# Kernel optimization log

Measured on AMD Instinct MI355X. Metric: run time of the kernel, lower is better.

The kernel has to match this reference:

```python
import jax, jax.numpy as jnp
import numpy as np

B, L, D_MODEL, H, M = 16, 512, 512, 8, 2
E = D_MODEL // H      # d_keys = d_values = 64
KMA = 25              # series-decomp moving-average kernel
KLAM = 7              # lambda conv kernel in TrendRefinement
PI = float(np.pi)


def _diff_matrix(n):
    # first-order difference matrix, shape (n-1, n)
    D = np.zeros((n - 1, n), dtype=np.float32)
    D[:, 1:] += np.eye(n - 1, dtype=np.float32)
    D[:, :-1] -= np.eye(n - 1, dtype=np.float32)
    return D


def setup_inputs() -> dict:
    key = jax.random.key(0)
    ks = jax.random.split(key, 16)
    w = lambda k, shape, s=0.02: s * jax.random.normal(k, shape, dtype=jnp.float32)
    # TrendRefinement buffers: U,S from SVD of (D2^T D2), D2 = D_{L-1} @ D_L (second difference)
    D2 = _diff_matrix(L - 1) @ _diff_matrix(L)
    U, S, _ = np.linalg.svd(D2.T @ D2)
    return {
        'queries': jax.random.normal(ks[0], (B, L, D_MODEL), dtype=jnp.float32),
        'keys':    jax.random.normal(ks[1], (B, L, D_MODEL), dtype=jnp.float32),
        'values':  jax.random.normal(ks[2], (B, L, D_MODEL), dtype=jnp.float32),
        'Wq': w(ks[3], (D_MODEL, H * E)), 'bq': jnp.zeros((H * E,), jnp.float32),
        'Wk': w(ks[4], (D_MODEL, H * E)), 'bk': jnp.zeros((H * E,), jnp.float32),
        'Wv': w(ks[5], (D_MODEL, H * E)), 'bv': jnp.zeros((H * E,), jnp.float32),
        'Wqo': w(ks[6], (D_MODEL, M * H)), 'bqo': jnp.zeros((M * H,), jnp.float32),
        'Wko': w(ks[7], (D_MODEL, M * H)), 'bko': jnp.zeros((M * H,), jnp.float32),
        'Wqt': w(ks[8], (D_MODEL, M * H)), 'bqt': jnp.zeros((M * H,), jnp.float32),
        'Wkt': w(ks[9], (D_MODEL, M * H)), 'bkt': jnp.zeros((M * H,), jnp.float32),
        'Wo': w(ks[10], (H * E, D_MODEL)), 'bo': jnp.zeros((D_MODEL,), jnp.float32),
        'Wlam': w(ks[11], (1, E, KLAM), 0.1), 'blam': jnp.zeros((1,), jnp.float32),
        'U': jnp.asarray(U, dtype=jnp.float32),
        'S': jnp.asarray(S, dtype=jnp.float32),
    }


def _mov_avg(x):
    # x: (B, L, H, E); replicate-pad then window mean of size KMA, stride 1
    pad = (KMA - 1) // 2
    xp = jnp.concatenate([jnp.repeat(x[:, :1], pad, axis=1), x,
                          jnp.repeat(x[:, -1:], pad, axis=1)], axis=1)
    c = jnp.cumsum(xp, axis=1)
    c = jnp.concatenate([jnp.zeros_like(c[:, :1]), c], axis=1)
    return (c[:, KMA:] - c[:, :-KMA]) / jnp.float32(KMA)


def _forward(queries, keys, values, Wq, bq, Wk, bk, Wv, bv, Wqo, bqo, Wko, bko,
             Wqt, bqt, Wkt, bkt, Wo, bo, Wlam, blam, U, S):
    # phase (omega/theta) projections: kernel-1 Conv1d == pointwise linear
    q_om = jax.nn.relu(queries @ Wqo + bqo).reshape(B, L, H, M)
    k_om = jax.nn.relu(keys @ Wko + bko).reshape(B, L, H, M)
    q_th = jnp.tanh(queries @ Wqt + bqt).reshape(B, L, H, M) * PI
    k_th = jnp.tanh(keys @ Wkt + bkt).reshape(B, L, H, M) * PI

    q = (queries @ Wq + bq).reshape(B, L, H, E)
    k = (keys @ Wk + bk).reshape(B, L, H, E)
    v = (values @ Wv + bv).reshape(B, L, H, E)

    # series decomposition: keep residual, keep value trend
    q = q - _mov_avg(q)
    k = k - _mov_avg(k)
    v_trend = _mov_avg(v)
    v = v - v_trend

    # inner attention: periodic-rotation-modulated softmax attention
    t = jnp.arange(L, dtype=jnp.float32)[None, :, None, None]

    def rot(x, om, th):
        phase = om * t + th                                     # (B,L,H,M)
        c, s = jnp.cos(phase), jnp.sin(phase)
        xr = jnp.concatenate([x[..., None, :] * c[..., None],
                              x[..., None, :] * s[..., None]], axis=-1)  # (B,L,H,M,2E)
        return xr.reshape(B, L, H, 2 * M * E)

    qr = rot(q, q_om, q_th)
    kr = rot(k, k_om, k_th)
    scores = jnp.einsum('blhd,bshd->bhls', qr, kr) / jnp.sqrt(jnp.float32(E))
    attn = jax.nn.softmax(scores, axis=-1)
    out = jnp.einsum('bhls,bshd->blhd', attn, v)

    # trend refinement: per-(b,h) filter g = U diag(1/(1+lambda*S)) U^T
    pad = (KLAM - 1) // 2
    vt = v_trend.transpose(0, 2, 3, 1).reshape(B * H, E, L)
    vtp = jnp.pad(vt, ((0, 0), (0, 0), (pad, pad)), mode='edge')
    lam = jax.lax.conv_general_dilated(vtp, Wlam, (1,), 'VALID',
                                       dimension_numbers=('NCH', 'OIH', 'NCH'))
    lam = lam + blam[None, :, None]
    lambdas = 1.0 + jax.nn.elu(lam).reshape(B, H, L)            # lambdas[b,h,l]
    s_scaled = lambdas * S[None, None, :]                        # (B,H,L)
    g = jnp.einsum('il,bhl,jl->bhij', U, 1.0 / (1.0 + s_scaled), U)
    out = out + jnp.einsum('bhij,bjhd->bihd', g, v_trend)

    out = out.reshape(B, L, H * E) @ Wo + bo

    # smoothness penalties
    Dq = jnp.asarray(_diff_matrix(L))
    om_pen = (jnp.sum(jnp.einsum('ji,bihm->bjhm', Dq, q_om) ** 2)
              + jnp.sum(jnp.einsum('ji,bihm->bjhm', Dq, k_om) ** 2))
    th_pen = jnp.sum(q_th ** 2) + jnp.sum(k_th ** 2)
    return out, attn, om_pen, th_pen


def reference(queries, keys, values, Wq, bq, Wk, bk, Wv, bv, Wqo, bqo, Wko, bko,
              Wqt, bqt, Wkt, bkt, Wo, bo, Wlam, blam, U, S):
    return _forward(queries, keys, values, Wq, bq, Wk, bk, Wv, bv, Wqo, bqo,
                    Wko, bko, Wqt, bqt, Wkt, bkt, Wo, bo, Wlam, blam, U, S)
```

## Files before the change

kernel.cpp:

```cpp
#include <hip/hip_runtime.h>
#include <math.h>


#define PI_F 3.14159265358979323846f

typedef __attribute__((ext_vector_type(8))) short bf16x8;
typedef __attribute__((ext_vector_type(4))) float f32x4;

static constexpr long ATTN_OFF = 4194304;
static constexpr long OM_OFF   = 37748736;
static constexpr long TH_OFF   = 37748737;

__device__ __forceinline__ ushort f2bf(float f){
  uint u = __float_as_uint(f);
  u += 0x7fffu + ((u >> 16) & 1u);
  return (ushort)(u >> 16);
}
__device__ __forceinline__ float bf2f(ushort h){
  return __uint_as_float((uint)h << 16);
}
__device__ __forceinline__ uint4 cvt8s(const float* f){
  ushort h[8];
#pragma unroll
  for (int j = 0; j < 8; j++) h[j] = f2bf(f[j]);
  uint4 H;
  H.x = (uint)h[0] | ((uint)h[1] << 16); H.y = (uint)h[2] | ((uint)h[3] << 16);
  H.z = (uint)h[4] | ((uint)h[5] << 16); H.w = (uint)h[6] | ((uint)h[7] << 16);
  return H;
}

template<int ROWS>
__device__ __forceinline__ void stage_sb(const short* __restrict__ G, int ldk,
                                         short* dst, int t){
#pragma unroll
  for (int i = 0; i < ROWS*8/256; i++){
    int p = t + i*256;
    int row = p >> 3;
    int kb = (p & 7) ^ (row & 7);
    __builtin_amdgcn_global_load_lds(
        (const __attribute__((address_space(1))) uint*)(G + (long)row*ldk + kb*8),
        (__attribute__((address_space(3))) uint*)(dst + (long)p*8), 16, 0, 0);
  }
}

template<int ROWS>
__device__ __forceinline__ void stage_sync(const short* __restrict__ G, int ldk,
                                           short* dst, int t){
#pragma unroll
  for (int i = 0; i < ROWS*8/256; i++){
    int p = t + i*256;
    int row = p >> 3, kb = p & 7;
    uint4 v = *(const uint4*)(G + (long)row*ldk + kb*8);
    *(uint4*)&dst[row*64 + ((kb ^ (row & 7)) << 3)] = v;
  }
}

template<int BM,int BN,bool QKV,int EPI>
__global__ __launch_bounds__(256)
void mgemm(int K,
  const short* __restrict__ AB, int lda, long sAb, long sAh,
  const short* __restrict__ BB, long sBb, long sBh,
  float* __restrict__ C, int ldc, long sCb, long sCh,
  const float* __restrict__ bias, const float* __restrict__ bias1, const float* __restrict__ bias2,
  const float* __restrict__ wcolp, short* __restrict__ CB, int Hdiv)
{
  __shared__ short As[BM*64], Bs[BN*64];
  constexpr int WMT = BM/2, WNT = BN/2;
  constexpr int FM = WMT/16, FN = WNT/16;

  const int z = blockIdx.z;
  const int zb = z / Hdiv, zh = z % Hdiv;
  const short* Ab = AB;
  const short* Bb = BB;
  float* Cb = C;
  short* Cbb = CB;
  if constexpr (QKV){
    Ab += (long)zb*4194304;
    if constexpr (EPI >= 4) Cbb += (long)zb*4194304;
  } else {
    Ab += (long)zb*sAb + (long)zh*sAh;
    Bb += (long)zb*sBb + (long)zh*sBh;
    if (C) Cb += (long)zb*sCb + (long)zh*sCh;
    if constexpr (EPI >= 4) Cbb += (long)zb*sCb + (long)zh*sCh;
  }

  const int t = threadIdx.x;
  const int m0 = blockIdx.y*BM, n0 = blockIdx.x*BN;
  const int wave = t >> 6, lane = t & 63;
  const int wr = wave >> 1, wc = wave & 1;
  const int lr = lane & 15, lk = lane >> 4;

  f32x4 acc[FM][FN];
#pragma unroll
  for (int mi = 0; mi < FM; mi++)
#pragma unroll
    for (int nj = 0; nj < FN; nj++) acc[mi][nj] = (f32x4){0.f, 0.f, 0.f, 0.f};

  for (int k0 = 0; k0 < K; k0 += 64){
    stage_sb<BM>(Ab + (long)m0*lda + k0, lda, As, t);
    stage_sb<BN>(Bb + (long)n0*K + k0, K, Bs, t);
    __syncthreads();
#pragma unroll
    for (int kk = 0; kk < 2; kk++){
      bf16x8 ah[FM], bh[FN];
#pragma unroll
      for (int mi = 0; mi < FM; mi++){
        int row = wr*WMT + mi*16 + lr;
        ah[mi] = *(const bf16x8*)&As[row*64 + (((kk*4 + lk) ^ (row & 7)) << 3)];
      }
#pragma unroll
      for (int nj = 0; nj < FN; nj++){
        int col = wc*WNT + nj*16 + lr;
        bh[nj] = *(const bf16x8*)&Bs[col*64 + (((kk*4 + lk) ^ (col & 7)) << 3)];
      }
#pragma unroll
      for (int mi = 0; mi < FM; mi++)
#pragma unroll
        for (int nj = 0; nj < FN; nj++)
          acc[mi][nj] = __builtin_amdgcn_mfma_f32_16x16x32_bf16(ah[mi], bh[nj], acc[mi][nj], 0, 0, 0);
    }
    __syncthreads();
  }

  const float* wz = nullptr;
  if constexpr (EPI == 4) wz = wcolp + (long)z*512;
  const float* bp = bias;
  if constexpr (QKV) bp = (zb == 0) ? bias : ((zb == 1) ? bias1 : bias2);

#pragma unroll
  for (int mi = 0; mi < FM; mi++){
#pragma unroll
    for (int r = 0; r < 4; r++){
      int grow = m0 + wr*WMT + mi*16 + lk*4 + r;
#pragma unroll
      for (int nj = 0; nj < FN; nj++){
        int gcol = n0 + wc*WNT + nj*16 + lr;
        float v = acc[mi][nj][r];
        if constexpr (EPI == 1 || EPI == 6) v += bp[gcol];
        if constexpr (EPI == 5) v += Cb[(long)grow*ldc + gcol];
        if constexpr (EPI == 4) v *= wz[gcol];
        if constexpr (EPI >= 4) Cbb[(long)grow*ldc + gcol] = (short)f2bf(v);
        else                    Cb[(long)grow*ldc + gcol] = v;
      }
    }
  }
}

__global__ __launch_bounds__(256)
void wconv_t(const float* __restrict__ W0, const float* __restrict__ W1,
             const float* __restrict__ W2, const float* __restrict__ W3,
             short* B0, short* B1, short* B2, short* B3)
{
  const float* W; short* Bp;
  switch (blockIdx.z){
    case 0:  W = W0; Bp = B0; break;
    case 1:  W = W1; Bp = B1; break;
    case 2:  W = W2; Bp = B2; break;
    default: W = W3; Bp = B3; break;
  }
  __shared__ float s[64][65];
  const int r0 = blockIdx.y*64, c0 = blockIdx.x*64;
  const int t = threadIdx.x;
#pragma unroll
  for (int i = 0; i < 4; i++){
    int idx = t + i*256;
    int r = idx >> 4, c4 = (idx & 15)*4;
    float4 v = *(const float4*)(W + (long)(r0 + r)*512 + c0 + c4);
    s[r][c4+0] = v.x; s[r][c4+1] = v.y; s[r][c4+2] = v.z; s[r][c4+3] = v.w;
  }
  __syncthreads();
#pragma unroll
  for (int i = 0; i < 2; i++){
    int p = t + i*256;
    int n = p >> 3, kb = p & 7;
    float f[8];
#pragma unroll
    for (int j = 0; j < 8; j++) f[j] = s[kb*8 + j][n];
    *(uint4*)&Bp[(long)(c0 + n)*512 + r0 + kb*8] = cvt8s(f);
  }
}

__global__ __launch_bounds__(256)
void uconv(const float* __restrict__ U, short* __restrict__ UB, short* __restrict__ UtB)
{
  __shared__ float s[64][65];
  const int r0 = blockIdx.y*64, c0 = blockIdx.x*64;
  const int t = threadIdx.x;
#pragma unroll
  for (int i = 0; i < 4; i++){
    int idx = t + i*256;
    int r = idx >> 4, c4 = (idx & 15)*4;
    float4 v = *(const float4*)(U + (long)(r0 + r)*512 + c0 + c4);
    s[r][c4+0] = v.x; s[r][c4+1] = v.y; s[r][c4+2] = v.z; s[r][c4+3] = v.w;
  }
  __syncthreads();
#pragma unroll
  for (int i = 0; i < 2; i++){
    int p = t + i*256;
    int rr = p >> 3, kb = p & 7;
    float f[8];
#pragma unroll
    for (int j = 0; j < 8; j++) f[j] = s[rr][kb*8 + j];
    *(uint4*)&UB[(long)(r0 + rr)*512 + c0 + kb*8] = cvt8s(f);
  }
#pragma unroll
  for (int i = 0; i < 2; i++){
    int p = t + i*256;
    int n = p >> 3, kb = p & 7;
    float f[8];
#pragma unroll
    for (int j = 0; j < 8; j++) f[j] = s[kb*8 + j][n];
    *(uint4*)&UtB[(long)(c0 + n)*512 + r0 + kb*8] = cvt8s(f);
  }
}

__global__ __launch_bounds__(256)
void acvt(const float* __restrict__ q, const float* __restrict__ k,
          const float* __restrict__ v, short* __restrict__ base)
{
  long g = (long)blockIdx.x*256 + threadIdx.x;
  if (g >= 1572864) return;
  long idx = g & 524287; int sel = (int)(g >> 19);
  const float* src = sel == 0 ? q : (sel == 1 ? k : v);
  short* Bp = base + (long)sel*4194304;
  float f[8];
  *(float4*)&f[0] = *(const float4*)(src + idx*8);
  *(float4*)&f[4] = *(const float4*)(src + idx*8 + 4);
  *(uint4*)&Bp[idx*8] = cvt8s(f);
}

__global__ __launch_bounds__(256)
void skinny_k(const float* __restrict__ Xq, const float* __restrict__ Xk,
              const float* __restrict__ Wqo, const float* __restrict__ bqo,
              const float* __restrict__ Wqt, const float* __restrict__ bqt,
              const float* __restrict__ Wko, const float* __restrict__ bko,
              const float* __restrict__ Wkt, const float* __restrict__ bkt,
              float* __restrict__ q_om, float* __restrict__ q_th, float* __restrict__ Cq,
              float* __restrict__ k_om, float* __restrict__ k_th, float* __restrict__ Ck)
{
    const int sel = blockIdx.y;
    const float* X   = sel ? Xk  : Xq;
    const float* Wom = sel ? Wko : Wqo;  const float* bom = sel ? bko : bqo;
    const float* Wth = sel ? Wkt : Wqt;  const float* bth = sel ? bkt : bqt;
    float* om_out = sel ? k_om : q_om;
    float* th_out = sel ? k_th : q_th;
    float* Cph    = sel ? Ck   : Cq;

    const int t = threadIdx.x;
    const int tx = t & 31, ty = t >> 5;
    const long row = (long)blockIdx.x * 8 + ty;
    const int col = tx & 15;
    const bool isTh = tx >= 16;
    const float* __restrict__ Wm = isTh ? Wth : Wom;
    const float* __restrict__ xr = X + row * 512;
    float acc0 = 0.f, acc1 = 0.f, acc2 = 0.f, acc3 = 0.f;
    for (int k = 0; k < 512; k += 4) {
        acc0 += xr[k + 0] * Wm[(k + 0) * 16 + col];
        acc1 += xr[k + 1] * Wm[(k + 1) * 16 + col];
        acc2 += xr[k + 2] * Wm[(k + 2) * 16 + col];
        acc3 += xr[k + 3] * Wm[(k + 3) * 16 + col];
    }
    float acc = (acc0 + acc1) + (acc2 + acc3);
    __shared__ float som[8][16], sth[8][16];
    float res;
    if (isTh) {
        res = tanhf(acc + bth[col]) * PI_F;
        th_out[row * 16 + col] = res;
        sth[ty][col] = res;
    } else {
        res = fmaxf(acc + bom[col], 0.f);
        om_out[row * 16 + col] = res;
        som[ty][col] = res;
    }
    __syncthreads();
    if (t < 64){
        const int r2 = t >> 3, h = t & 7;
        const long grow = (long)blockIdx.x * 8 + r2;
        const float tt = (float)(grow & 511);
        const float o0 = som[r2][h*2], o1 = som[r2][h*2+1];
        const float t0 = sth[r2][h*2], t1 = sth[r2][h*2+1];
        float c0, s0, c1, s1;
        sincosf(o0 * tt + t0, &s0, &c0);
        sincosf(o1 * tt + t1, &s1, &c1);
        float4 rr = { c0, s0, c1, s1 };
        *(float4*)&Cph[grow * 32 + h * 4] = rr;
    }
}

__global__ __launch_bounds__(256)
void movavg_all(const short* __restrict__ qpB, const short* __restrict__ kpB,
                const short* __restrict__ vpB,
                short* __restrict__ qRB, short* __restrict__ kRB,
                short* __restrict__ VTB, short* __restrict__ TTB)
{
    const int zz = blockIdx.z;
    const int src = zz >> 4, b = zz & 15;
    const int l0 = blockIdx.y * 64, c0 = blockIdx.x * 64;
    const short* XB = src == 0 ? qpB : (src == 1 ? kpB : vpB);
    short* RB = src == 0 ? qRB : kRB;
    __shared__ float sm[88][64];
    const long base = (long)b * 512 * 512 + c0;
    const int t = threadIdx.x;
    for (int i = t; i < 88 * 64; i += 256) {
        const int r = i >> 6, c = i & 63;
        int gl = l0 + r - 12;
        gl = min(max(gl, 0), 511);
        sm[r][c] = bf2f((ushort)XB[base + (long)gl * 512 + c]);
    }
    __syncthreads();
    const int tx = t & 63, ty = t >> 6;
    const int rbase = ty * 16;
    float s = 0.f;
    #pragma unroll
    for (int d = 0; d < 25; d++) s += sm[rbase + d][tx];
    const float inv = 1.f / 25.f;
    short hb[16], tb[16];
    #pragma unroll
    for (int r = 0; r < 16; r++) {
        const long l = l0 + rbase + r;
        const float ma = s * inv;
        const float x = sm[rbase + r + 12][tx];
        const float res = x - ma;
        if (src < 2) {
            RB[((long)b * 512 + l) * 512 + c0 + tx] = (short)f2bf(res);
        } else {
            hb[r] = (short)f2bf(res);
            tb[r] = (short)f2bf(ma);
        }
        if (r < 15) s += sm[rbase + r + 25][tx] - sm[rbase + r][tx];
    }
    if (src == 2) {
        const long vo = ((long)b * 512 + c0 + tx) * 512 + l0 + rbase;
        *(uint4*)&VTB[vo]     = ((uint4*)hb)[0];
        *(uint4*)&VTB[vo + 8] = ((uint4*)hb)[1];
        *(uint4*)&TTB[vo]     = ((uint4*)tb)[0];
        *(uint4*)&TTB[vo + 8] = ((uint4*)tb)[1];
    }
}

__global__ __launch_bounds__(256)
void flash_k(const short* __restrict__ qB, const short* __restrict__ kB,
             const short* __restrict__ vtB,
             const float* __restrict__ Cq, const float* __restrict__ Ck,
             float* __restrict__ attn, float* __restrict__ attn_out)
{
  const int bid = blockIdx.y*8 + blockIdx.x;
  const int swz = (bid & 7)*128 + (bid >> 3);
  const int z = swz >> 3; const int b = z >> 3, h = z & 7;
  const int l0 = (swz & 7) * 64;
  const int t = threadIdx.x, wave = t >> 6, lane = t & 63;
  const int lr = lane & 15, lk = lane >> 4;

  __shared__ short SH[8192];
  __shared__ float CkS[2048];
  short* Qs = SH;
  short* Ks = SH;
  short* PPs = SH;
  short* Vs = SH + 4096;

  const int sr0 = t >> 3,          skb0 = t & 7;
  const int sr1 = (t >> 3) + 32,   skb1 = t & 7;
  const int sidx0 = sr0*64 + ((skb0 ^ (sr0 & 7)) << 3);
  const int sidx1 = sr1*64 + ((skb1 ^ (sr1 & 7)) << 3);

  stage_sync<64>(qB + ((long)(b*512 + l0))*512 + h*64, 512, Qs, t);
#pragma unroll
  for (int i = 0; i < 2; i++){
    int s = t + i*256;
    ((float4*)CkS)[s] = *(const float4*)(Ck + (((long)b*512 + s)*8 + h)*4);
  }
  __syncthreads();
  bf16x8 aq[2];
#pragma unroll
  for (int kk = 0; kk < 2; kk++){
    int row = wave*16 + lr;
    aq[kk] = *(const bf16x8*)&Qs[row*64 + (((kk*4 + lk) ^ (row & 7)) << 3)];
  }

  const long kbase0 = ((long)(b*512 + sr0))*512 + h*64 + skb0*8;
  const long kbase1 = ((long)(b*512 + sr1))*512 + h*64 + skb1*8;
  uint4 pA0, pA1, pB0, pB1;
  pA0 = *(const uint4*)(kB + kbase0);
  pA1 = *(const uint4*)(kB + kbase1);
  __syncthreads();

  f32x4 acc[32];
#pragma unroll
  for (int a = 0; a < 32; a++) acc[a] = (f32x4){0.f,0.f,0.f,0.f};
#pragma unroll
  for (int st = 0; st < 8; st++){
    if (st & 1){
      *(uint4*)&Ks[sidx0] = pB0; *(uint4*)&Ks[sidx1] = pB1;
      if (st < 7){
        pA0 = *(const uint4*)(kB + kbase0 + (long)(st+1)*64*512);
        pA1 = *(const uint4*)(kB + kbase1 + (long)(st+1)*64*512);
      }
    } else {
      *(uint4*)&Ks[sidx0] = pA0; *(uint4*)&Ks[sidx1] = pA1;
      if (st < 7){
        pB0 = *(const uint4*)(kB + kbase0 + (long)(st+1)*64*512);
        pB1 = *(const uint4*)(kB + kbase1 + (long)(st+1)*64*512);
      }
    }
    __syncthreads();
#pragma unroll
    for (int nj = 0; nj < 4; nj++){
      int srow = nj*16 + lr;
#pragma unroll
      for (int kk = 0; kk < 2; kk++){
        bf16x8 bh = *(const bf16x8*)&Ks[srow*64 + (((kk*4 + lk) ^ (srow & 7)) << 3)];
        acc[st*4+nj] = __builtin_amdgcn_mfma_f32_16x16x32_bf16(aq[kk], bh, acc[st*4+nj], 0,0,0);
      }
    }
    if (st < 7) __syncthreads();
  }

  const long vbase0 = ((long)(z*64 + sr0))*512 + skb0*8;
  const long vbase1 = ((long)(z*64 + sr1))*512 + skb1*8;
  pA0 = *(const uint4*)(vtB + vbase0);
  pA1 = *(const uint4*)(vtB + vbase1);

  float4 cqv[4];
#pragma unroll
  for (int r = 0; r < 4; r++){
    int row = l0 + wave*16 + lk*4 + r;
    cqv[r] = *(const float4*)(Cq + (((long)b*512 + row)*8 + h)*4);
  }
#pragma unroll
  for (int a = 0; a < 32; a++){
    int col = (a >> 2)*64 + (a & 3)*16 + lr;
    float4 ckv = ((float4*)CkS)[col];
#pragma unroll
    for (int r = 0; r < 4; r++){
      float mod = 0.125f*(cqv[r].x*ckv.x + cqv[r].y*ckv.y + cqv[r].z*ckv.z + cqv[r].w*ckv.w);
      acc[a][r] *= mod;
    }
  }
  float mx[4] = {-INFINITY, -INFINITY, -INFINITY, -INFINITY};
#pragma unroll
  for (int a = 0; a < 32; a++)
#pragma unroll
    for (int r = 0; r < 4; r++) mx[r] = fmaxf(mx[r], acc[a][r]);
#pragma unroll
  for (int msk = 1; msk < 16; msk <<= 1)
#pragma unroll
    for (int r = 0; r < 4; r++) mx[r] = fmaxf(mx[r], __shfl_xor(mx[r], msk));
  float sme[4] = {0.f, 0.f, 0.f, 0.f};
#pragma unroll
  for (int a = 0; a < 32; a++)
#pragma unroll
    for (int r = 0; r < 4; r++){ float e = __expf(acc[a][r] - mx[r]); acc[a][r] = e; sme[r] += e; }
#pragma unroll
  for (int msk = 1; msk < 16; msk <<= 1)
#pragma unroll
    for (int r = 0; r < 4; r++) sme[r] += __shfl_xor(sme[r], msk);
  float inv[4];
#pragma unroll
  for (int r = 0; r < 4; r++) inv[r] = 1.f / sme[r];
#pragma unroll
  for (int a = 0; a < 32; a++)
#pragma unroll
    for (int r = 0; r < 4; r++) acc[a][r] *= inv[r];

  f32x4 oacc[4];
#pragma unroll
  for (int nj = 0; nj < 4; nj++) oacc[nj] = (f32x4){0.f,0.f,0.f,0.f};
#pragma unroll
  for (int st = 0; st < 8; st++){
    __syncthreads();
#pragma unroll
    for (int a2 = 0; a2 < 4; a2++){
      int c = a2*16 + lr;
#pragma unroll
      for (int r = 0; r < 4; r++){
        int row = wave*16 + lk*4 + r;
        PPs[row*64 + (((c >> 3) ^ (row & 7)) << 3) + (c & 7)] = (short)f2bf(acc[st*4+a2][r]);
      }
    }
    if (st & 1){
      *(uint4*)&Vs[sidx0] = pB0; *(uint4*)&Vs[sidx1] = pB1;
      if (st < 7){
        pA0 = *(const uint4*)(vtB + vbase0 + (st+1)*64);
        pA1 = *(const uint4*)(vtB + vbase1 + (st+1)*64);
      }
    } else {
      *(uint4*)&Vs[sidx0] = pA0; *(uint4*)&Vs[sidx1] = pA1;
      if (st < 7){
        pB0 = *(const uint4*)(vtB + vbase0 + (st+1)*64);
        pB1 = *(const uint4*)(vtB + vbase1 + (st+1)*64);
      }
    }
#pragma unroll
    for (int a2 = 0; a2 < 4; a2++){
      int col = st*64 + a2*16 + lr;
#pragma unroll
      for (int r = 0; r < 4; r++)
        attn[((long)z*512 + l0 + wave*16 + lk*4 + r)*512 + col] = acc[st*4+a2][r];
    }
    __syncthreads();
#pragma unroll
    for (int kk = 0; kk < 2; kk++){
      int prow = wave*16 + lr;
      int phys = (kk*4 + lk) ^ (prow & 7);
      bf16x8 ah = *(const bf16x8*)&PPs[prow*64 + phys*8];
#pragma unroll
      for (int nj = 0; nj < 4; nj++){
        int vrow = nj*16 + lr;
        bf16x8 bh = *(const bf16x8*)&Vs[vrow*64 + (((kk*4 + lk) ^ (vrow & 7)) << 3)];
        oacc[nj] = __builtin_amdgcn_mfma_f32_16x16x32_bf16(ah, bh, oacc[nj], 0,0,0);
      }
    }
  }
#pragma unroll
  for (int nj = 0; nj < 4; nj++)
#pragma unroll
    for (int r = 0; r < 4; r++){
      int grow = l0 + wave*16 + lk*4 + r;
      attn_out[((long)b*512 + grow)*512 + h*64 + nj*16 + lr] = oacc[nj][r];
    }
}

__global__ __launch_bounds__(512)
void lamw_k(const short* __restrict__ TTB, const float* __restrict__ Wlam,
            const float* __restrict__ blam, const float* __restrict__ Sv,
            float* __restrict__ Wout)
{
    const int z = blockIdx.x;
    const int b = z >> 3, h = z & 7;
    __shared__ float sv[512][17];
    __shared__ float sw[448];
    const int t = threadIdx.x;
    if (t < 448) sw[t] = Wlam[t];
    const short* __restrict__ Tb = TTB + ((long)b * 512 + h * 64) * 512;
    float lam = 0.f;
    for (int ec = 0; ec < 4; ec++) {
        __syncthreads();
        #pragma unroll
        for (int j = 0; j < 16; j++)
            sv[t][j] = bf2f((ushort)Tb[(long)(ec * 16 + j) * 512 + t]);
        __syncthreads();
        #pragma unroll
        for (int dk = 0; dk < 7; dk++) {
            int r = t + dk - 3;
            r = min(max(r, 0), 511);
            #pragma unroll
            for (int j = 0; j < 16; j++)
                lam += sv[r][j] * sw[(ec * 16 + j) * 7 + dk];
        }
    }
    lam += blam[0];
    const float el = lam > 0.f ? lam : expm1f(lam);
    const float wv = 1.f / (1.f + (1.f + el) * Sv[t]);
    Wout[(long)z * 512 + t] = wv;
}

__global__ __launch_bounds__(256)
void pen1_k(const float* __restrict__ qom, const float* __restrict__ kom,
            const float* __restrict__ qth, const float* __restrict__ kth,
            float* __restrict__ partials)
{
    const long tid = (long)blockIdx.x * 256 + threadIdx.x;
    float om = 0.f, th = 0.f;
    for (long i = tid; i < 262144; i += 65536) {
        const float* om_arr = (i < 131072) ? qom : kom;
        const float* th_arr = (i < 131072) ? qth : kth;
        const long j = i & 131071;
        const float x = th_arr[j];
        th += x * x;
        const int l = (int)((j >> 4) & 511);
        if (l < 511) {
            const float d = om_arr[j + 16] - om_arr[j];
            om += d * d;
        }
    }
    __shared__ float som[256], sth[256];
    som[threadIdx.x] = om; sth[threadIdx.x] = th;
    __syncthreads();
    for (int o = 128; o; o >>= 1) {
        if (threadIdx.x < o) {
            som[threadIdx.x] += som[threadIdx.x + o];
            sth[threadIdx.x] += sth[threadIdx.x + o];
        }
        __syncthreads();
    }
    if (threadIdx.x == 0) {
        partials[blockIdx.x] = som[0];
        partials[256 + blockIdx.x] = sth[0];
    }
}

__global__ __launch_bounds__(256)
void pen2_k(const float* __restrict__ partials, float* __restrict__ om_out,
            float* __restrict__ th_out)
{
    __shared__ float som[256], sth[256];
    const int t = threadIdx.x;
    som[t] = partials[t]; sth[t] = partials[256 + t];
    __syncthreads();
    for (int o = 128; o; o >>= 1) {
        if (t < o) { som[t] += som[t + o]; sth[t] += sth[t + o]; }
        __syncthreads();
    }
    if (t == 0) { *om_out = som[0]; *th_out = sth[0]; }
}

extern "C" void kernel_launch(void* const* d_in, const int* in_sizes, int n_in,
                              void* d_out_v, int out_size, void* d_ws, size_t ws_size,
                              hipStream_t stream)
{
    const float* queries = (const float*)d_in[0];
    const float* keys    = (const float*)d_in[1];
    const float* values  = (const float*)d_in[2];
    const float* Wq  = (const float*)d_in[3];  const float* bq  = (const float*)d_in[4];
    const float* Wk  = (const float*)d_in[5];  const float* bk  = (const float*)d_in[6];
    const float* Wv  = (const float*)d_in[7];  const float* bv  = (const float*)d_in[8];
    const float* Wqo = (const float*)d_in[9];  const float* bqo = (const float*)d_in[10];
    const float* Wko = (const float*)d_in[11]; const float* bko = (const float*)d_in[12];
    const float* Wqt = (const float*)d_in[13]; const float* bqt = (const float*)d_in[14];
    const float* Wkt = (const float*)d_in[15]; const float* bkt = (const float*)d_in[16];
    const float* Wo  = (const float*)d_in[17]; const float* bo  = (const float*)d_in[18];
    const float* Wlam= (const float*)d_in[19]; const float* blam= (const float*)d_in[20];
    const float* U   = (const float*)d_in[21]; const float* Sv  = (const float*)d_in[22];

    float* out = (float*)d_out_v;
    float* W   = (float*)d_ws;

    short* qpB = (short*)W;
    short* kpB = (short*)(W + 4194304);
    short* vpB = (short*)(W + 8388608);
    float* attn_out = W + 4194304;
    short* TTB = (short*)(W + 12582912);
    short* R1  = (short*)(W + 16777216);
    short* qinB = R1;
    short* kinB = R1 + 4194304;
    short* vinB = R1 + 8388608;
    short* qresB = qinB;  short* kresB = kinB;  short* vtB = vinB;
    short* aoB = kresB;
    short* T1tB = (short*)W;
    short* UB  = (short*)(W + 8388608);
    short* UtB = UB + 262144;
    float* q_om = W + 29360128;
    float* k_om = q_om + 131072;
    float* q_th = k_om + 131072;
    float* k_th = q_th + 131072;
    float* Cq   = k_th + 131072;
    float* Ck   = Cq + 262144;
    float* wbuf = Ck + 262144;
    float* partials = wbuf + 65536;
    short* wsp = (short*)(W + 30475264);
    short* WqB = wsp;
    short* WkB = wsp + 262144;
    short* WvB = wsp + 524288;
    short* WoB = wsp + 786432;

    float* attn = out + ATTN_OFF;
    dim3 blk(256);

    wconv_t<<<dim3(8,8,4), blk, 0, stream>>>(Wq, Wk, Wv, Wo, WqB, WkB, WvB, WoB);
    acvt<<<dim3(6144), blk, 0, stream>>>(queries, keys, values, R1);

    mgemm<128,128,true,6><<<dim3(4,64,3), blk, 0, stream>>>(
        512, qinB, 512, 0, 0, WqB, 0, 0,
        nullptr, 512, 0, 0,
        bq, bk, bv, nullptr, qpB, 1);

    skinny_k<<<dim3(1024,2), blk, 0, stream>>>(queries, keys,
        Wqo, bqo, Wqt, bqt, Wko, bko, Wkt, bkt,
        q_om, q_th, Cq, k_om, k_th, Ck);

    movavg_all<<<dim3(8,8,48), blk, 0, stream>>>(qpB, kpB, vpB,
        qresB, kresB, vtB, TTB);

    uconv<<<dim3(8,8), blk, 0, stream>>>(U, UB, UtB);

    flash_k<<<dim3(8,128), blk, 0, stream>>>(qresB, kresB, vtB, Cq, Ck, attn, attn_out);

    lamw_k<<<dim3(128), dim3(512), 0, stream>>>(TTB, Wlam, blam, Sv, wbuf);

    mgemm<64,128,false,4><<<dim3(4,1,128), blk, 0, stream>>>(
        512, TTB, 512, 262144, 32768, UtB, 0, 0,
        nullptr, 512, 262144, 32768,
        nullptr, nullptr, nullptr, wbuf, T1tB, 8);

    mgemm<128,64,false,5><<<dim3(1,4,128), blk, 0, stream>>>(
        512, UB, 512, 0, 0, T1tB, 262144, 32768,
        attn_out, 512, 262144, 64,
        nullptr, nullptr, nullptr, nullptr, aoB, 8);

    mgemm<64,128,false,1><<<dim3(4,128,1), blk, 0, stream>>>(
        512, aoB, 512, 0, 0, WoB, 0, 0,
        out, 512, 0, 0,
        bo, nullptr, nullptr, nullptr, nullptr, 1);

    pen1_k<<<dim3(256), blk, 0, stream>>>(q_om, k_om, q_th, k_th, partials);
    pen2_k<<<dim3(1), blk, 0, stream>>>(partials, out + OM_OFF, out + TH_OFF);
}
```

Baseline: 240.1 us.

## Double-buffer K/P/V tiles in LDS with 128-wide stages and MFMA priority

The flash attention kernel now processes keys and values in four stages of 128 instead of eight of 64. K, P and V tiles are double-buffered in LDS, which removes one barrier per stage, and the swizzle moves from the LDS write side to the global read side. s_setprio is raised around the MFMA loops. LDS use grows from about 24KB to about 72KB per block, which may reduce occupancy, and more prefetch registers are live.

```diff
diff --git a/kernel.cpp b/kernel.cpp
--- a/kernel.cpp
+++ b/kernel.cpp
@@ -351,17 +351,15 @@
   const int t = threadIdx.x, wave = t >> 6, lane = t & 63;
   const int lr = lane & 15, lk = lane >> 4;
 
-  __shared__ short SH[8192];
+  __shared__ short SH[32768];
   __shared__ float CkS[2048];
-  short* Qs = SH;
-  short* Ks = SH;
-  short* PPs = SH;
-  short* Vs = SH + 4096;
-
-  const int sr0 = t >> 3,          skb0 = t & 7;
-  const int sr1 = (t >> 3) + 32,   skb1 = t & 7;
-  const int sidx0 = sr0*64 + ((skb0 ^ (sr0 & 7)) << 3);
-  const int sidx1 = sr1*64 + ((skb1 ^ (sr1 & 7)) << 3);
+  short* Qs  = SH;
+  short* Ks0 = SH;
+  short* Ks1 = SH + 8192;
+  short* PP0 = SH;
+  short* PP1 = SH + 8192;
+  short* Vs0 = SH + 16384;
+  short* Vs1 = SH + 24576;
 
   stage_sync<64>(qB + ((long)(b*512 + l0))*512 + h*64, 512, Qs, t);
 #pragma unroll
@@ -377,48 +375,65 @@
     aq[kk] = *(const bf16x8*)&Qs[row*64 + (((kk*4 + lk) ^ (row & 7)) << 3)];
   }
 
-  const long kbase0 = ((long)(b*512 + sr0))*512 + h*64 + skb0*8;
-  const long kbase1 = ((long)(b*512 + sr1))*512 + h*64 + skb1*8;
-  uint4 pA0, pA1, pB0, pB1;
-  pA0 = *(const uint4*)(kB + kbase0);
-  pA1 = *(const uint4*)(kB + kbase1);
+  int sidx[4]; long kgoff[4];
+  uint4 pA0,pA1,pA2,pA3, pB0,pB1,pB2,pB3;
+#pragma unroll
+  for (int i = 0; i < 4; i++){
+    int p = t + i*256;
+    int row = p >> 3, kb = p & 7;
+    sidx[i] = p*8;
+    kgoff[i] = ((long)(b*512 + row))*512 + h*64 + ((kb ^ (row & 7))*8);
+  }
+  pA0 = *(const uint4*)(kB + kgoff[0]); pA1 = *(const uint4*)(kB + kgoff[1]);
+  pA2 = *(const uint4*)(kB + kgoff[2]); pA3 = *(const uint4*)(kB + kgoff[3]);
   __syncthreads();
 
   f32x4 acc[32];
 #pragma unroll
   for (int a = 0; a < 32; a++) acc[a] = (f32x4){0.f,0.f,0.f,0.f};
 #pragma unroll
-  for (int st = 0; st < 8; st++){
+  for (int st = 0; st < 4; st++){
+    short* Kcur = (st & 1) ? Ks1 : Ks0;
     if (st & 1){
-      *(uint4*)&Ks[sidx0] = pB0; *(uint4*)&Ks[sidx1] = pB1;
-      if (st < 7){
-        pA0 = *(const uint4*)(kB + kbase0 + (long)(st+1)*64*512);
-        pA1 = *(const uint4*)(kB + kbase1 + (long)(st+1)*64*512);
+      *(uint4*)&Kcur[sidx[0]] = pB0; *(uint4*)&Kcur[sidx[1]] = pB1;
+      *(uint4*)&Kcur[sidx[2]] = pB2; *(uint4*)&Kcur[sidx[3]] = pB3;
+      if (st < 3){
+        long o = (long)(st+1)*128*512;
+        pA0 = *(const uint4*)(kB + kgoff[0] + o); pA1 = *(const uint4*)(kB + kgoff[1] + o);
+        pA2 = *(const uint4*)(kB + kgoff[2] + o); pA3 = *(const uint4*)(kB + kgoff[3] + o);
       }
     } else {
-      *(uint4*)&Ks[sidx0] = pA0; *(uint4*)&Ks[sidx1] = pA1;
-      if (st < 7){
-        pB0 = *(const uint4*)(kB + kbase0 + (long)(st+1)*64*512);
-        pB1 = *(const uint4*)(kB + kbase1 + (long)(st+1)*64*512);
+      *(uint4*)&Kcur[sidx[0]] = pA0; *(uint4*)&Kcur[sidx[1]] = pA1;
+      *(uint4*)&Kcur[sidx[2]] = pA2; *(uint4*)&Kcur[sidx[3]] = pA3;
+      if (st < 3){
+        long o = (long)(st+1)*128*512;
+        pB0 = *(const uint4*)(kB + kgoff[0] + o); pB1 = *(const uint4*)(kB + kgoff[1] + o);
+        pB2 = *(const uint4*)(kB + kgoff[2] + o); pB3 = *(const uint4*)(kB + kgoff[3] + o);
       }
     }
     __syncthreads();
-#pragma unroll
-    for (int nj = 0; nj < 4; nj++){
+    __builtin_amdgcn_s_setprio(1);
+#pragma unroll
+    for (int nj = 0; nj < 8; nj++){
       int srow = nj*16 + lr;
 #pragma unroll
       for (int kk = 0; kk < 2; kk++){
-        bf16x8 bh = *(const bf16x8*)&Ks[srow*64 + (((kk*4 + lk) ^ (srow & 7)) << 3)];
-        acc[st*4+nj] = __builtin_amdgcn_mfma_f32_16x16x32_bf16(aq[kk], bh, acc[st*4+nj], 0,0,0);
-      }
-    }
-    if (st < 7) __syncthreads();
-  }
-
-  const long vbase0 = ((long)(z*64 + sr0))*512 + skb0*8;
-  const long vbase1 = ((long)(z*64 + sr1))*512 + skb1*8;
-  pA0 = *(const uint4*)(vtB + vbase0);
-  pA1 = *(const uint4*)(vtB + vbase1);
+        bf16x8 bh = *(const bf16x8*)&Kcur[srow*64 + (((kk*4 + lk) ^ (srow & 7)) << 3)];
+        acc[st*8+nj] = __builtin_amdgcn_mfma_f32_16x16x32_bf16(aq[kk], bh, acc[st*8+nj], 0,0,0);
+      }
+    }
+    __builtin_amdgcn_s_setprio(0);
+  }
+
+  long vgoff[4];
+#pragma unroll
+  for (int i = 0; i < 4; i++){
+    int p = t + i*256;
+    int row = p >> 4, sb = p & 15;
+    vgoff[i] = ((long)(z*64 + row))*512 + ((sb ^ (row & 15))*8);
+  }
+  pA0 = *(const uint4*)(vtB + vgoff[0]); pA1 = *(const uint4*)(vtB + vgoff[1]);
+  pA2 = *(const uint4*)(vtB + vgoff[2]); pA3 = *(const uint4*)(vtB + vgoff[3]);
 
   float4 cqv[4];
 #pragma unroll
@@ -428,7 +443,7 @@
   }
 #pragma unroll
   for (int a = 0; a < 32; a++){
-    int col = (a >> 2)*64 + (a & 3)*16 + lr;
+    int col = (a >> 3)*128 + (a & 7)*16 + lr;
     float4 ckv = ((float4*)CkS)[col];
 #pragma unroll
     for (int r = 0; r < 4; r++){
@@ -466,50 +481,59 @@
 #pragma unroll
   for (int nj = 0; nj < 4; nj++) oacc[nj] = (f32x4){0.f,0.f,0.f,0.f};
 #pragma unroll
-  for (int st = 0; st < 8; st++){
-    __syncthreads();
-#pragma unroll
-    for (int a2 = 0; a2 < 4; a2++){
+  for (int st = 0; st < 4; st++){
+    short* Pcur = (st & 1) ? PP1 : PP0;
+    short* Vcur = (st & 1) ? Vs1 : Vs0;
+#pragma unroll
+    for (int a2 = 0; a2 < 8; a2++){
       int c = a2*16 + lr;
+      int cb = c >> 3;
 #pragma unroll
       for (int r = 0; r < 4; r++){
         int row = wave*16 + lk*4 + r;
-        PPs[row*64 + (((c >> 3) ^ (row & 7)) << 3) + (c & 7)] = (short)f2bf(acc[st*4+a2][r]);
+        Pcur[row*128 + ((cb ^ (row & 15)) << 3) + (c & 7)] = (short)f2bf(acc[st*8+a2][r]);
       }
     }
     if (st & 1){
-      *(uint4*)&Vs[sidx0] = pB0; *(uint4*)&Vs[sidx1] = pB1;
-      if (st < 7){
-        pA0 = *(const uint4*)(vtB + vbase0 + (st+1)*64);
-        pA1 = *(const uint4*)(vtB + vbase1 + (st+1)*64);
+      *(uint4*)&Vcur[sidx[0]] = pB0; *(uint4*)&Vcur[sidx[1]] = pB1;
+      *(uint4*)&Vcur[sidx[2]] = pB2; *(uint4*)&Vcur[sidx[3]] = pB3;
+      if (st < 3){
+        long o = (st+1)*128;
+        pA0 = *(const uint4*)(vtB + vgoff[0] + o); pA1 = *(const uint4*)(vtB + vgoff[1] + o);
+        pA2 = *(const uint4*)(vtB + vgoff[2] + o); pA3 = *(const uint4*)(vtB + vgoff[3] + o);
       }
     } else {
-      *(uint4*)&Vs[sidx0] = pA0; *(uint4*)&Vs[sidx1] = pA1;
-      if (st < 7){
-        pB0 = *(const uint4*)(vtB + vbase0 + (st+1)*64);
-        pB1 = *(const uint4*)(vtB + vbase1 + (st+1)*64);
-      }
-    }
-#pragma unroll
-    for (int a2 = 0; a2 < 4; a2++){
-      int col = st*64 + a2*16 + lr;
+      *(uint4*)&Vcur[sidx[0]] = pA0; *(uint4*)&Vcur[sidx[1]] = pA1;
+      *(uint4*)&Vcur[sidx[2]] = pA2; *(uint4*)&Vcur[sidx[3]] = pA3;
+      if (st < 3){
+        long o = (st+1)*128;
+        pB0 = *(const uint4*)(vtB + vgoff[0] + o); pB1 = *(const uint4*)(vtB + vgoff[1] + o);
+        pB2 = *(const uint4*)(vtB + vgoff[2] + o); pB3 = *(const uint4*)(vtB + vgoff[3] + o);
+      }
+    }
+#pragma unroll
+    for (int a2 = 0; a2 < 8; a2++){
+      int col = st*128 + a2*16 + lr;
 #pragma unroll
       for (int r = 0; r < 4; r++)
-        attn[((long)z*512 + l0 + wave*16 + lk*4 + r)*512 + col] = acc[st*4+a2][r];
+        attn[((long)z*512 + l0 + wave*16 + lk*4 + r)*512 + col] = acc[st*8+a2][r];
     }
     __syncthreads();
-#pragma unroll
-    for (int kk = 0; kk < 2; kk++){
+    __builtin_amdgcn_s_setprio(1);
+#pragma unroll
+    for (int kk = 0; kk < 4; kk++){
       int prow = wave*16 + lr;
-      int phys = (kk*4 + lk) ^ (prow & 7);
-      bf16x8 ah = *(const bf16x8*)&PPs[prow*64 + phys*8];
+      int phys = (kk*4 + lk) ^ (prow & 15);
+      bf16x8 ah = *(const bf16x8*)&Pcur[prow*128 + phys*8];
 #pragma unroll
       for (int nj = 0; nj < 4; nj++){
         int vrow = nj*16 + lr;
-        bf16x8 bh = *(const bf16x8*)&Vs[vrow*64 + (((kk*4 + lk) ^ (vrow & 7)) << 3)];
+        int vphys = (kk*4 + lk) ^ (vrow & 15);
+        bf16x8 bh = *(const bf16x8*)&Vcur[vrow*128 + vphys*8];
         oacc[nj] = __builtin_amdgcn_mfma_f32_16x16x32_bf16(ah, bh, oacc[nj], 0,0,0);
       }
     }
+    __builtin_amdgcn_s_setprio(0);
   }
 #pragma unroll
   for (int nj = 0; nj < 4; nj++)
```

Result: no change. 237.9 us (-0.9%).
